# Kernel tuning notes

Measured on AMD Instinct MI355X. Metric: run time of the kernel, lower is better.

The kernel has to match this reference:

```python
import jax, jax.numpy as jnp
import numpy as np

B, DIN, N = 8, 256, 2048  # batch, input_dim (orig node_num), attention nodes (orig seq_len)


def setup_inputs() -> dict:
    key = jax.random.key(0)
    k1, k2, k3, k4 = jax.random.split(key, 4)
    x = jax.random.normal(k1, (B, DIN, N), jnp.float32)
    adj = jax.random.randint(k2, (N, N), 0, 2).astype(jnp.int32)  # binary adjacency
    W = jax.random.normal(k3, (DIN, DIN), jnp.float32) * 0.05      # Linear(D, D, bias=False), stored (out, in)
    a = jax.random.normal(k4, (3 * DIN,), jnp.float32) * 0.05      # Linear(3D, 1, bias=False)
    return {"x": x, "adj": adj, "W": W, "a": a}


def reference(x, adj, W, a):
    # x: (B, D, N) -> permute to (B, N, D); attention is over the N axis
    xt = jnp.transpose(x, (0, 2, 1))
    h = xt @ W.T                                   # (B, N, D)
    sim = jnp.einsum('bid,bjd->bij', h, h)         # (B, N, N) pairwise dot products
    n = adj.shape[0]
    # neighbor mask: adj nonzero, diagonal forced off (mask[:, i] = 0 in the loop)
    m = (adj != 0) & (~jnp.eye(n, dtype=bool))
    # context: the torch loop's weighted_h is independent of its k axis, so
    # context[b, k, i, d] == C[b, i, d] = sum_j m[i,j] * sim[b,i,j] * h[b,j,d]
    C = jnp.einsum('bij,bjd->bid', jnp.where(m[None, :, :], sim, 0.0), h)  # (B, N, D)
    d = h.shape[-1]
    a1, a2, a3 = a[:d], a[d:2 * d], a[2 * d:]
    # a([h_i, h_j, C_j]) = a1.h_i + a2.h_j + a3.C_j  (concat never materialized)
    s_i = h @ a1                                   # (B, N)
    s_j = h @ a2 + C @ a3                          # (B, N)
    scores = jax.nn.leaky_relu(s_i[:, :, None] + s_j[:, None, :], negative_slope=0.2)
    scores = jnp.where(adj[None, :, :] == 0, jnp.float32(-9e15), scores)
    return jax.nn.softmax(scores, axis=-1)         # (B, N, N)
```

## Files before the change

kernel.cpp:

```cpp
#include <hip/hip_runtime.h>
#include <hip/hip_bf16.h>
#include <math.h>

#define Bq   8
#define DINq 256
#define Nq   2048

typedef __attribute__((ext_vector_type(8))) short bf16x8v;
typedef __attribute__((ext_vector_type(4))) float f32x4v;

__device__ __forceinline__ unsigned short f2bf(float f) {
  union { float f; unsigned u; } v; v.f = f;
  unsigned r = v.u + 0x7fffu + ((v.u >> 16) & 1u);
  return (unsigned short)(r >> 16);
}
__device__ __forceinline__ float bf2f(unsigned short h) {
  union { unsigned u; float f; } v; v.u = ((unsigned)h) << 16;
  return v.f;
}

__device__ __forceinline__ void gld_lds16(const void* g, void* l) {
  __builtin_amdgcn_global_load_lds(
      (const __attribute__((address_space(1))) unsigned int*)g,
      (__attribute__((address_space(3))) unsigned int*)l, 16, 0, 0);
}

__device__ __forceinline__ bf16x8v expand_mask(unsigned m8) {
  union { unsigned u[4]; bf16x8v v; } r;
  unsigned lo4 = ((m8 & 0xFu) * 0x204081u) & 0x01010101u;
  unsigned hi4 = (((m8 >> 4) & 0xFu) * 0x204081u) & 0x01010101u;
  r.u[0] = ((lo4 & 0xFFu) | ((lo4 & 0xFF00u) << 8)) * 0x3F80u;
  r.u[1] = (((lo4 >> 16) & 0xFFu) | ((lo4 >> 24) << 16)) * 0x3F80u;
  r.u[2] = ((hi4 & 0xFFu) | ((hi4 & 0xFF00u) << 8)) * 0x3F80u;
  r.u[3] = (((hi4 >> 16) & 0xFFu) | ((hi4 >> 24) << 16)) * 0x3F80u;
  return r.v;
}

__global__ void k_prep(const float* __restrict__ W, const float* __restrict__ a,
                       float* __restrict__ w123) {
  __shared__ float red[3][4][256];
  const int k = threadIdx.x & 255, dq = threadIdx.x >> 8;
  float s1 = 0.f, s2 = 0.f, s3 = 0.f;
  for (int d = dq * 64; d < dq * 64 + 64; ++d) {
    float w = W[d * DINq + k];
    s1 += w * a[d];
    s2 += w * a[DINq + d];
    s3 += w * a[2 * DINq + d];
  }
  red[0][dq][k] = s1; red[1][dq][k] = s2; red[2][dq][k] = s3;
  __syncthreads();
  if (threadIdx.x < 256) {
    w123[k]            = red[0][0][k] + red[0][1][k] + red[0][2][k] + red[0][3][k];
    w123[DINq + k]     = red[1][0][k] + red[1][1][k] + red[1][2][k] + red[1][3][k];
    w123[2 * DINq + k] = red[2][0][k] + red[2][1][k] + red[2][2][k] + red[2][3][k];
  }
}

__global__ void k_transposeW(const float* __restrict__ W, float* __restrict__ WT) {
  int d = blockIdx.x, k = threadIdx.x;
  WT[(size_t)k * DINq + d] = W[(size_t)d * DINq + k];
}

__global__ __launch_bounds__(256, 2) void k_hX(const float* __restrict__ x,
                     const float* __restrict__ WT, const float* __restrict__ w123,
                     unsigned short* __restrict__ Xhi, unsigned short* __restrict__ Xlo,
                     float* __restrict__ tA, float* __restrict__ siA,
                     float* __restrict__ sbA) {
  __shared__ float xs[64][32];
  __shared__ float ws[64][256];
  __shared__ float wls[768];
  __shared__ float Tt[32];
  const int tid = threadIdx.x;
  const int iq = tid & 7;
  const int dg = tid >> 3;
  const int i0 = blockIdx.x * 32;
  const int b = blockIdx.y;
  const int lane = tid & 63;
  const bool w0 = (tid < 64);
  const int ti = lane & 31;
  const int khalf = (lane >> 5) * 32;

  for (int n = tid; n < 768; n += 256) wls[n] = w123[n];

  float acc[4][8];
#pragma unroll
  for (int e = 0; e < 4; ++e)
#pragma unroll
    for (int cc = 0; cc < 8; ++cc) acc[e][cc] = 0.f;
  float p1 = 0.f, p2 = 0.f, p3 = 0.f;

  for (int kc = 0; kc < 4; ++kc) {
    __syncthreads();
#pragma unroll
    for (int l = 0; l < 2; ++l) {
      int c = l * 256 + tid;
      int r = c >> 3, ch = c & 7;
      gld_lds16(&x[((size_t)b * DINq + kc * 64 + r) * Nq + i0 + ch * 4], &xs[r][ch * 4]);
    }
#pragma unroll
    for (int l = 0; l < 16; ++l) {
      int c = l * 256 + tid;
      int r = c >> 6, ch = c & 63;
      gld_lds16(&WT[(size_t)(kc * 64 + r) * DINq + ch * 4], &ws[r][ch * 4]);
    }
    asm volatile("s_waitcnt vmcnt(0)" ::: "memory");
    __syncthreads();
#pragma unroll 4
    for (int kk = 0; kk < 64; ++kk) {
      f32x4v xv = *(const f32x4v*)&xs[kk][iq * 4];
      f32x4v wv0 = *(const f32x4v*)&ws[kk][dg * 8];
      f32x4v wv1 = *(const f32x4v*)&ws[kk][dg * 8 + 4];
#pragma unroll
      for (int e = 0; e < 4; ++e) {
#pragma unroll
        for (int cc = 0; cc < 4; ++cc) {
          acc[e][cc]     += xv[e] * wv0[cc];
          acc[e][cc + 4] += xv[e] * wv1[cc];
        }
      }
    }
    if (w0) {
#pragma unroll 4
      for (int k2 = 0; k2 < 32; ++k2) {
        int kk = khalf + k2;
        float xv = xs[kk][ti];
        p1 += xv * wls[kc * 64 + kk];
        p2 += xv * wls[256 + kc * 64 + kk];
        p3 += xv * wls[512 + kc * 64 + kk];
      }
    }
  }

  if (w0) {
    p1 += __shfl_xor(p1, 32, 64);
    p2 += __shfl_xor(p2, 32, 64);
    p3 += __shfl_xor(p3, 32, 64);
    if (lane < 32) {
      Tt[lane] = p3;
      tA[(size_t)b * Nq + i0 + lane] = p3;
      siA[(size_t)b * Nq + i0 + lane] = p1;
      sbA[(size_t)b * Nq + i0 + lane] = p2;
    }
  }
  __syncthreads();

  float tv[4];
#pragma unroll
  for (int e = 0; e < 4; ++e) tv[e] = Tt[iq * 4 + e];

#pragma unroll
  for (int cc = 0; cc < 8; ++cc) {
    const int d = dg * 8 + cc;
    unsigned short hv[4], lv[4];
#pragma unroll
    for (int e = 0; e < 4; ++e) {
      float Xv = tv[e] * acc[e][cc];
      unsigned short hs = f2bf(Xv);
      hv[e] = hs;
      lv[e] = f2bf(Xv - bf2f(hs));
    }
    size_t off = ((size_t)b * DINq + d) * Nq + i0 + iq * 4;
    *(ushort4*)&Xhi[off] = make_ushort4(hv[0], hv[1], hv[2], hv[3]);
    *(ushort4*)&Xlo[off] = make_ushort4(lv[0], lv[1], lv[2], lv[3]);
  }
}

__global__ void k_mask(const int* __restrict__ adj, unsigned* __restrict__ bm) {
  int wg = blockIdx.x * 256 + threadIdx.x;
  int i = wg >> 6, w = wg & 63, j0 = w * 32;
  const int4* ap = (const int4*)&adj[(size_t)i * Nq + j0];
  unsigned bits = 0;
#pragma unroll
  for (int q = 0; q < 8; ++q) {
    int4 a = ap[q];
    if (a.x) bits |= 1u << (q * 4);
    if (a.y) bits |= 1u << (q * 4 + 1);
    if (a.z) bits |= 1u << (q * 4 + 2);
    if (a.w) bits |= 1u << (q * 4 + 3);
  }
  bm[wg] = bits;
}

__global__ __launch_bounds__(256, 4) void k_gemm(const unsigned* __restrict__ bm,
                                                 const unsigned short* __restrict__ Xhi,
                                                 const unsigned short* __restrict__ Xlo,
                                                 float* __restrict__ sjp) {
  __shared__ __align__(16) unsigned short Bs[3][128 * 32];
  __shared__ unsigned bmlds[128 * 16];
  __shared__ float swb[4][64];
  const int tid = threadIdx.x;
  const int lane = tid & 63;
  const int wave = tid >> 6;
  const int wm = wave >> 1, wc = wave & 1;
  const int wg = blockIdx.x;
  const int xcd = wg & 7;
  const int sub = wg >> 3;
  const int ct = xcd * 2 + (sub & 1);
  const int mt = (sub >> 1) & 15;
  const int ks = sub >> 5;
  const int i0 = mt * 128, c0 = ct * 128, kbase = ks * 512;
  const int r15 = lane & 15, kg = lane >> 4;
  const int kb = 16 * (kg ^ ((r15 >> 1) & 3));

  {
    const int kw0 = kbase >> 5;
#pragma unroll
    for (int n = 0; n < 2; ++n) {
      int idx4 = n * 256 + tid;
      int r = idx4 >> 2, w4 = (idx4 & 3) * 4;
      uint4 v = *(const uint4*)&bm[(size_t)(i0 + r) * 64 + kw0 + w4];
      bmlds[r * 16 + ((w4 + 0) ^ (r & 15))] = v.x;
      bmlds[r * 16 + ((w4 + 1) ^ (r & 15))] = v.y;
      bmlds[r * 16 + ((w4 + 2) ^ (r & 15))] = v.z;
      bmlds[r * 16 + ((w4 + 3) ^ (r & 15))] = v.w;
    }
  }
  __syncthreads();

  f32x4v acc[4][4];
#pragma unroll
  for (int m = 0; m < 4; ++m)
#pragma unroll
    for (int n = 0; n < 4; ++n) acc[m][n] = (f32x4v)0.f;

  auto STAGE = [&](int buf, int t) {
    const unsigned short* __restrict__ src = (t & 1) ? Xlo : Xhi;
    const int k0 = kbase + (t >> 1) * 32;
#pragma unroll
    for (int l = 0; l < 2; ++l) {
      const int pc = l * 256 + tid;
      const int row = pc >> 2, q = pc & 3;
      const int kc = 8 * (q ^ ((row >> 1) & 3));
      gld_lds16(&src[(size_t)(c0 + row) * Nq + k0 + kc], &Bs[buf][pc * 8]);
    }
  };

  constexpr int NT = 32;
  STAGE(0, 0);
  STAGE(1, 1);
  int cb = 0, sb2 = 2;
  for (int t = 0; t < NT; ++t) {
    if (t + 1 < NT) {
      asm volatile("s_waitcnt vmcnt(2)" ::: "memory");
    } else {
      asm volatile("s_waitcnt vmcnt(0)" ::: "memory");
    }
    __builtin_amdgcn_sched_barrier(0);
    __builtin_amdgcn_s_barrier();
    __builtin_amdgcn_sched_barrier(0);
    if (t + 2 < NT) STAGE(sb2, t + 2);

    const char* Bb = (const char*)&Bs[cb][0];
    bf16x8v bf[4];
#pragma unroll
    for (int n = 0; n < 4; ++n)
      bf[n] = *(const bf16x8v*)(Bb + (wc * 64 + n * 16 + r15) * 64 + kb);
    const int kch = t >> 1;
    const int jb = kbase + kch * 32 + kg * 8;
#pragma unroll
    for (int m = 0; m < 4; ++m) {
      const int arow = wm * 64 + m * 16 + r15;
      unsigned wv = bmlds[arow * 16 + (kch ^ (arow & 15))];
      unsigned m8 = (wv >> (kg * 8)) & 0xFFu;
      unsigned d = (unsigned)(i0 + arow - jb);
      if (d < 8u) m8 &= ~(1u << d);
      bf16x8v af = expand_mask(m8);
      __builtin_amdgcn_s_setprio(1);
#pragma unroll
      for (int n = 0; n < 4; ++n)
        acc[m][n] = __builtin_amdgcn_mfma_f32_16x16x32_bf16(af, bf[n], acc[m][n], 0, 0, 0);
      __builtin_amdgcn_s_setprio(0);
    }
    cb = (cb == 2) ? 0 : cb + 1;
    sb2 = (sb2 == 2) ? 0 : sb2 + 1;
  }

  const int b = c0 >> 8;
  const int re = (lane >> 4) * 4, ce = lane & 15;
  float s[4][4];
#pragma unroll
  for (int m = 0; m < 4; ++m)
#pragma unroll
    for (int r = 0; r < 4; ++r) s[m][r] = 0.f;
#pragma unroll
  for (int n = 0; n < 4; ++n) {
    const size_t xrow = (size_t)(c0 + wc * 64 + n * 16 + ce) * Nq;
#pragma unroll
    for (int m = 0; m < 4; ++m) {
      const size_t ib = xrow + i0 + wm * 64 + m * 16 + re;
      ushort4 xh = *(const ushort4*)&Xhi[ib];
      ushort4 xl = *(const ushort4*)&Xlo[ib];
      s[m][0] += acc[m][n][0] * (bf2f(xh.x) + bf2f(xl.x));
      s[m][1] += acc[m][n][1] * (bf2f(xh.y) + bf2f(xl.y));
      s[m][2] += acc[m][n][2] * (bf2f(xh.z) + bf2f(xl.z));
      s[m][3] += acc[m][n][3] * (bf2f(xh.w) + bf2f(xl.w));
    }
  }
#pragma unroll
  for (int o = 1; o < 16; o <<= 1) {
#pragma unroll
    for (int m = 0; m < 4; ++m)
#pragma unroll
      for (int r = 0; r < 4; ++r) s[m][r] += __shfl_xor(s[m][r], o, 64);
  }
  if (ce == 0) {
#pragma unroll
    for (int m = 0; m < 4; ++m)
#pragma unroll
      for (int r = 0; r < 4; ++r)
        swb[wave][m * 16 + re + r] = s[m][r];
  }
  __builtin_amdgcn_s_barrier();
  {
    const int slice = (ct & 1) * 8 + ks * 2 + wc;
    float* sp = sjp + ((size_t)slice * Bq + b) * Nq + i0 + wm * 64;
    sp[lane] = swb[wave][lane];
  }
}

__global__ void k_sjsum(const float* __restrict__ sbA, const float* __restrict__ tA,
                        const float* __restrict__ sjp, float* __restrict__ sjvA) {
  int idx = blockIdx.x * 256 + threadIdx.x;
  float s = 0.f;
#pragma unroll
  for (int sl = 0; sl < 16; ++sl) s += sjp[(size_t)sl * Bq * Nq + idx];
  sjvA[idx] = sbA[idx] + s / tA[idx];
}

__global__ void k_softmax(const unsigned* __restrict__ bm, const float* __restrict__ siA,
                          const float* __restrict__ sjvA, float* __restrict__ out) {
  const int b = blockIdx.y, i = blockIdx.x, tid = threadIdx.x;
  const float siv = siA[(size_t)b * Nq + i];
  const unsigned* brow = bm + (size_t)i * 64;
  const float* sjb = sjvA + (size_t)b * Nq;
  const int bit = tid & 31;
  float sc[8];
  float mx = -3.0e38f;
#pragma unroll
  for (int s = 0; s < 8; ++s) {
    int j = s * 256 + tid;
    float v = siv + sjb[j];
    v = v > 0.f ? v : 0.2f * v;
    unsigned wv = brow[j >> 5];
    v = ((wv >> bit) & 1u) ? v : -9.0e15f;
    sc[s] = v;
    mx = fmaxf(mx, v);
  }
#pragma unroll
  for (int o = 32; o >= 1; o >>= 1) mx = fmaxf(mx, __shfl_xor(mx, o, 64));
  __shared__ float redm[4], reds[4];
  const int wave = tid >> 6, lane = tid & 63;
  if (lane == 0) redm[wave] = mx;
  __syncthreads();
  mx = fmaxf(fmaxf(redm[0], redm[1]), fmaxf(redm[2], redm[3]));
  float sum = 0.f, ex[8];
#pragma unroll
  for (int s = 0; s < 8; ++s) { ex[s] = expf(sc[s] - mx); sum += ex[s]; }
#pragma unroll
  for (int o = 32; o >= 1; o >>= 1) sum += __shfl_xor(sum, o, 64);
  if (lane == 0) reds[wave] = sum;
  __syncthreads();
  sum = reds[0] + reds[1] + reds[2] + reds[3];
  float inv = 1.f / sum;
  float* orow = out + ((size_t)b * Nq + i) * Nq;
#pragma unroll
  for (int s = 0; s < 8; ++s) orow[s * 256 + tid] = ex[s] * inv;
}

extern "C" void kernel_launch(void* const* d_in, const int* in_sizes, int n_in,
                              void* d_out, int out_size, void* d_ws, size_t ws_size,
                              hipStream_t stream) {
  const float* x = (const float*)d_in[0];
  const int* adj = (const int*)d_in[1];
  const float* W = (const float*)d_in[2];
  const float* a = (const float*)d_in[3];
  float* out = (float*)d_out;

  char* ws = (char*)d_ws;
  size_t off = 0;
  auto alloc = [&](size_t bytes) -> void* {
    void* p = ws + off;
    off += (bytes + 255) & ~(size_t)255;
    return p;
  };
  float* w123 = (float*)alloc(3 * DINq * sizeof(float));
  float* WT = (float*)alloc((size_t)DINq * DINq * sizeof(float));
  float* tA = (float*)alloc((size_t)Bq * Nq * sizeof(float));
  float* siA = (float*)alloc((size_t)Bq * Nq * sizeof(float));
  float* sbA = (float*)alloc((size_t)Bq * Nq * sizeof(float));
  float* sjvA = (float*)alloc((size_t)Bq * Nq * sizeof(float));
  float* sjp = (float*)alloc((size_t)16 * Bq * Nq * sizeof(float));
  unsigned short* Xhi = (unsigned short*)alloc((size_t)Nq * Nq * 2);
  unsigned short* Xlo = (unsigned short*)alloc((size_t)Nq * Nq * 2);
  unsigned* bm = (unsigned*)alloc((size_t)Nq * 64 * sizeof(unsigned));

  k_prep<<<dim3(1), dim3(1024), 0, stream>>>(W, a, w123);
  k_transposeW<<<dim3(DINq), dim3(DINq), 0, stream>>>(W, WT);
  k_hX<<<dim3(Nq / 32, Bq), dim3(256), 0, stream>>>(x, WT, w123, Xhi, Xlo, tA, siA, sbA);
  k_mask<<<dim3(Nq * 64 / 256), dim3(256), 0, stream>>>(adj, bm);
  k_gemm<<<dim3(1024), dim3(256), 0, stream>>>(bm, Xhi, Xlo, sjp);
  k_sjsum<<<dim3(Bq * Nq / 256), dim3(256), 0, stream>>>(sbA, tA, sjp, sjvA);
  k_softmax<<<dim3(Nq, Bq), dim3(256), 0, stream>>>(bm, siA, sjvA, out);
}
```

Measured before the change: 146.7 us.

## Double M tile in mask GEMM and fuse hi/lo loads per k-step

The mask GEMM now gives each workgroup a 256-row M tile instead of 128, halving the grid to 512 blocks. Each k-step stages the hi and lo bf16 halves together into a two-buffer pipeline. Every expanded mask fragment is then reused across both halves and twice as many B columns, cutting mask expansion and B-tile reloads per FLOP. The cost is more accumulator registers (occupancy hint lowered from 4 to 3), an extra barrier per iteration, and fewer blocks to fill the GPU.

```diff
diff --git a/kernel.cpp b/kernel.cpp
--- a/kernel.cpp
+++ b/kernel.cpp
@@ -181,13 +181,13 @@
   bm[wg] = bits;
 }
 
-__global__ __launch_bounds__(256, 4) void k_gemm(const unsigned* __restrict__ bm,
+__global__ __launch_bounds__(256, 3) void k_gemm(const unsigned* __restrict__ bm,
                                                  const unsigned short* __restrict__ Xhi,
                                                  const unsigned short* __restrict__ Xlo,
                                                  float* __restrict__ sjp) {
-  __shared__ __align__(16) unsigned short Bs[3][128 * 32];
-  __shared__ unsigned bmlds[128 * 16];
-  __shared__ float swb[4][64];
+  __shared__ __align__(16) unsigned short Bs[2][2][128 * 32];
+  __shared__ unsigned bmlds[256 * 16];
+  __shared__ float swb[4][128];
   const int tid = threadIdx.x;
   const int lane = tid & 63;
   const int wave = tid >> 6;
@@ -196,16 +196,16 @@
   const int xcd = wg & 7;
   const int sub = wg >> 3;
   const int ct = xcd * 2 + (sub & 1);
-  const int mt = (sub >> 1) & 15;
-  const int ks = sub >> 5;
-  const int i0 = mt * 128, c0 = ct * 128, kbase = ks * 512;
+  const int mt = (sub >> 1) & 7;
+  const int ks = sub >> 4;
+  const int i0 = mt * 256, c0 = ct * 128, kbase = ks * 512;
   const int r15 = lane & 15, kg = lane >> 4;
   const int kb = 16 * (kg ^ ((r15 >> 1) & 3));
 
   {
     const int kw0 = kbase >> 5;
 #pragma unroll
-    for (int n = 0; n < 2; ++n) {
+    for (int n = 0; n < 4; ++n) {
       int idx4 = n * 256 + tid;
       int r = idx4 >> 2, w4 = (idx4 & 3) * 4;
       uint4 v = *(const uint4*)&bm[(size_t)(i0 + r) * 64 + kw0 + w4];
@@ -217,77 +217,80 @@
   }
   __syncthreads();
 
-  f32x4v acc[4][4];
-#pragma unroll
-  for (int m = 0; m < 4; ++m)
+  f32x4v acc[8][4];
+#pragma unroll
+  for (int m = 0; m < 8; ++m)
 #pragma unroll
     for (int n = 0; n < 4; ++n) acc[m][n] = (f32x4v)0.f;
 
   auto STAGE = [&](int buf, int t) {
-    const unsigned short* __restrict__ src = (t & 1) ? Xlo : Xhi;
-    const int k0 = kbase + (t >> 1) * 32;
+    const int k0 = kbase + t * 32;
 #pragma unroll
     for (int l = 0; l < 2; ++l) {
       const int pc = l * 256 + tid;
       const int row = pc >> 2, q = pc & 3;
       const int kc = 8 * (q ^ ((row >> 1) & 3));
-      gld_lds16(&src[(size_t)(c0 + row) * Nq + k0 + kc], &Bs[buf][pc * 8]);
+      gld_lds16(&Xhi[(size_t)(c0 + row) * Nq + k0 + kc], &Bs[buf][0][pc * 8]);
+      gld_lds16(&Xlo[(size_t)(c0 + row) * Nq + k0 + kc], &Bs[buf][1][pc * 8]);
     }
   };
 
-  constexpr int NT = 32;
+  constexpr int NT = 16;
   STAGE(0, 0);
-  STAGE(1, 1);
-  int cb = 0, sb2 = 2;
+  int cb = 0;
   for (int t = 0; t < NT; ++t) {
     if (t + 1 < NT) {
-      asm volatile("s_waitcnt vmcnt(2)" ::: "memory");
+      STAGE(cb ^ 1, t + 1);
+      asm volatile("s_waitcnt vmcnt(4)" ::: "memory");
     } else {
       asm volatile("s_waitcnt vmcnt(0)" ::: "memory");
     }
     __builtin_amdgcn_sched_barrier(0);
     __builtin_amdgcn_s_barrier();
     __builtin_amdgcn_sched_barrier(0);
-    if (t + 2 < NT) STAGE(sb2, t + 2);
-
-    const char* Bb = (const char*)&Bs[cb][0];
-    bf16x8v bf[4];
-#pragma unroll
-    for (int n = 0; n < 4; ++n)
-      bf[n] = *(const bf16x8v*)(Bb + (wc * 64 + n * 16 + r15) * 64 + kb);
-    const int kch = t >> 1;
-    const int jb = kbase + kch * 32 + kg * 8;
-#pragma unroll
-    for (int m = 0; m < 4; ++m) {
-      const int arow = wm * 64 + m * 16 + r15;
-      unsigned wv = bmlds[arow * 16 + (kch ^ (arow & 15))];
+
+    const char* Bh = (const char*)&Bs[cb][0][0];
+    const char* Bl = (const char*)&Bs[cb][1][0];
+    bf16x8v bfh[4], bfl[4];
+#pragma unroll
+    for (int n = 0; n < 4; ++n) {
+      bfh[n] = *(const bf16x8v*)(Bh + (wc * 64 + n * 16 + r15) * 64 + kb);
+      bfl[n] = *(const bf16x8v*)(Bl + (wc * 64 + n * 16 + r15) * 64 + kb);
+    }
+    const int jb = kbase + t * 32 + kg * 8;
+#pragma unroll
+    for (int m = 0; m < 8; ++m) {
+      const int arow = wm * 128 + m * 16 + r15;
+      unsigned wv = bmlds[arow * 16 + (t ^ (arow & 15))];
       unsigned m8 = (wv >> (kg * 8)) & 0xFFu;
       unsigned d = (unsigned)(i0 + arow - jb);
       if (d < 8u) m8 &= ~(1u << d);
       bf16x8v af = expand_mask(m8);
       __builtin_amdgcn_s_setprio(1);
 #pragma unroll
-      for (int n = 0; n < 4; ++n)
-        acc[m][n] = __builtin_amdgcn_mfma_f32_16x16x32_bf16(af, bf[n], acc[m][n], 0, 0, 0);
+      for (int n = 0; n < 4; ++n) {
+        acc[m][n] = __builtin_amdgcn_mfma_f32_16x16x32_bf16(af, bfh[n], acc[m][n], 0, 0, 0);
+        acc[m][n] = __builtin_amdgcn_mfma_f32_16x16x32_bf16(af, bfl[n], acc[m][n], 0, 0, 0);
+      }
       __builtin_amdgcn_s_setprio(0);
     }
-    cb = (cb == 2) ? 0 : cb + 1;
-    sb2 = (sb2 == 2) ? 0 : sb2 + 1;
+    if (t + 1 < NT) __builtin_amdgcn_s_barrier();
+    cb ^= 1;
   }
 
   const int b = c0 >> 8;
   const int re = (lane >> 4) * 4, ce = lane & 15;
-  float s[4][4];
-#pragma unroll
-  for (int m = 0; m < 4; ++m)
+  float s[8][4];
+#pragma unroll
+  for (int m = 0; m < 8; ++m)
 #pragma unroll
     for (int r = 0; r < 4; ++r) s[m][r] = 0.f;
 #pragma unroll
   for (int n = 0; n < 4; ++n) {
     const size_t xrow = (size_t)(c0 + wc * 64 + n * 16 + ce) * Nq;
 #pragma unroll
-    for (int m = 0; m < 4; ++m) {
-      const size_t ib = xrow + i0 + wm * 64 + m * 16 + re;
+    for (int m = 0; m < 8; ++m) {
+      const size_t ib = xrow + i0 + wm * 128 + m * 16 + re;
       ushort4 xh = *(const ushort4*)&Xhi[ib];
       ushort4 xl = *(const ushort4*)&Xlo[ib];
       s[m][0] += acc[m][n][0] * (bf2f(xh.x) + bf2f(xl.x));
@@ -299,13 +302,13 @@
 #pragma unroll
   for (int o = 1; o < 16; o <<= 1) {
 #pragma unroll
-    for (int m = 0; m < 4; ++m)
+    for (int m = 0; m < 8; ++m)
 #pragma unroll
       for (int r = 0; r < 4; ++r) s[m][r] += __shfl_xor(s[m][r], o, 64);
   }
   if (ce == 0) {
 #pragma unroll
-    for (int m = 0; m < 4; ++m)
+    for (int m = 0; m < 8; ++m)
 #pragma unroll
       for (int r = 0; r < 4; ++r)
         swb[wave][m * 16 + re + r] = s[m][r];
@@ -313,8 +316,9 @@
   __builtin_amdgcn_s_barrier();
   {
     const int slice = (ct & 1) * 8 + ks * 2 + wc;
-    float* sp = sjp + ((size_t)slice * Bq + b) * Nq + i0 + wm * 64;
+    float* sp = sjp + ((size_t)slice * Bq + b) * Nq + i0 + wm * 128;
     sp[lane] = swb[wave][lane];
+    sp[64 + lane] = swb[wave][64 + lane];
   }
 }
 
@@ -398,7 +402,7 @@
   k_transposeW<<<dim3(DINq), dim3(DINq), 0, stream>>>(W, WT);
   k_hX<<<dim3(Nq / 32, Bq), dim3(256), 0, stream>>>(x, WT, w123, Xhi, Xlo, tA, siA, sbA);
   k_mask<<<dim3(Nq * 64 / 256), dim3(256), 0, stream>>>(adj, bm);
-  k_gemm<<<dim3(1024), dim3(256), 0, stream>>>(bm, Xhi, Xlo, sjp);
+  k_gemm<<<dim3(512), dim3(256), 0, stream>>>(bm, Xhi, Xlo, sjp);
   k_sjsum<<<dim3(Bq * Nq / 256), dim3(256), 0, stream>>>(sbA, tA, sjp, sjvA);
   k_softmax<<<dim3(Nq, Bq), dim3(256), 0, stream>>>(bm, siA, sjvA, out);
 }
```

Measured after the change: 167.2 us. 1.14x slower.
